# Optimization experiments

Measured on AMD Instinct MI355X. Metric: run time of the kernel, lower is better.

Reference implementation:

```python
import jax, jax.numpy as jnp
import numpy as np

# Renderer constants matching neural_renderer.Renderer(camera_mode='look',
# light_intensity_ambient=0.5, light_intensity_directional=0.5,
# light_direction=[0,0,1], viewing_angle=45) with image_size=256.
IMG = 256
TEX = 6
VIEW_ANGLE_DEG = 45.0
EYE = np.array([0.0, 0.0, -2.0], dtype=np.float32)          # camera position (look mode)
CAM_DIR = np.array([0.0, 0.0, 1.0], dtype=np.float32)       # camera_direction
CAM_UP = np.array([0.0, 1.0, 0.0], dtype=np.float32)        # camera_up
LIGHT_DIR = np.array([0.0, 0.0, 1.0], dtype=np.float32)
AMBIENT = 0.5
DIRECTIONAL = 0.5
EPS = 1e-8


def setup_inputs() -> dict:
    key = jax.random.key(0)
    k1, k2, k3 = jax.random.split(key, 3)
    # mesh roughly centered at origin; camera sits at z=-2 looking toward +z
    vertices = 0.5 * jax.random.normal(k1, (1, 400, 3), dtype=jnp.float32)
    faces = jax.random.randint(k2, (1, 640, 3), 0, 400, dtype=jnp.int64)
    textures = 0.5 * jax.random.normal(k3, (1, 640, TEX, TEX, TEX, 3), dtype=jnp.float32)
    return {"vertices": vertices, "faces": faces, "textures": textures}


def _normalize(v):
    return v / (jnp.linalg.norm(v, axis=-1, keepdims=True) + EPS)


def reference(vertices, faces, textures):
    v = vertices[0]                 # [N,3]
    f = faces[0]                    # [F,3] int
    tex = jnp.tanh(textures[0])     # [F,T,T,T,3]  (torch.tanh(textures))

    fv = v[f]                       # [F,3,3] per-face vertex positions (world)

    # ---- lighting (ambient + directional, white lights) ----
    n = jnp.cross(fv[:, 1] - fv[:, 0], fv[:, 2] - fv[:, 0])  # [F,3]
    n = _normalize(n)
    diff = jax.nn.relu(n @ jnp.asarray(LIGHT_DIR))           # [F]
    light = AMBIENT + DIRECTIONAL * diff                     # [F] (same for rgb)

    # ---- 'look' camera transform ----
    z_ax = _normalize(jnp.asarray(CAM_DIR))
    x_ax = _normalize(jnp.cross(jnp.asarray(CAM_UP), z_ax))
    y_ax = jnp.cross(z_ax, x_ax)
    R = jnp.stack([x_ax, y_ax, z_ax], axis=0)                # [3,3]
    vc = (fv - jnp.asarray(EYE)) @ R.T                       # [F,3,3] camera space

    # ---- perspective projection ----
    wfov = jnp.tan(jnp.deg2rad(VIEW_ANGLE_DEG)).astype(jnp.float32)
    zc = vc[..., 2]                                          # [F,3] depth
    xy = vc[..., :2] / (zc[..., None] * wfov + EPS)          # [F,3,2] in [-1,1]

    # ---- rasterize: barycentric coords per pixel per face ----
    ps = (jnp.arange(IMG, dtype=jnp.float32) + 0.5) / IMG * 2.0 - 1.0
    px, py = jnp.meshgrid(ps, -ps, indexing="xy")            # image y flipped
    pts = jnp.stack([px.ravel(), py.ravel()], axis=-1)       # [P,2]

    v0 = xy[:, 0]                                            # [F,2]
    d = xy[:, 1] - v0                                        # [F,2]
    e = xy[:, 2] - v0                                        # [F,2]
    det = d[:, 0] * e[:, 1] - d[:, 1] * e[:, 0]              # [F]
    det_ok = jnp.abs(det) > 1e-8
    det_s = jnp.where(det_ok, det, 1.0)

    q = pts[:, None, :] - v0[None, :, :]                     # [P,F,2]
    w1 = (q[..., 0] * e[:, 1] - q[..., 1] * e[:, 0]) / det_s # [P,F]
    w2 = (d[:, 0] * q[..., 1] - d[:, 1] * q[..., 0]) / det_s # [P,F]
    w0 = 1.0 - w1 - w2

    inside = (w0 >= 0) & (w1 >= 0) & (w2 >= 0) & det_ok[None, :]
    depth = w0 * zc[:, 0] + w1 * zc[:, 1] + w2 * zc[:, 2]    # [P,F]
    visible = inside & (depth > 0)

    # ---- z-buffer: nearest visible face per pixel ----
    big = jnp.float32(1e30)
    dmask = jnp.where(visible, depth, big)                   # [P,F]
    idx = jnp.argmin(dmask, axis=1)                          # [P]
    valid = jnp.take_along_axis(visible, idx[:, None], axis=1)[:, 0]  # [P]

    gather = lambda a: jnp.take_along_axis(a, idx[:, None], axis=1)[:, 0]
    b0, b1, b2 = gather(w0), gather(w1), gather(w2)          # [P] each

    # ---- texture lookup: nearest cell in TxTxT cube by barycentric coords ----
    ti = lambda b: jnp.clip((b * TEX).astype(jnp.int32), 0, TEX - 1)
    i0, i1, i2 = ti(b0), ti(b1), ti(b2)
    col = tex[idx, i0, i1, i2]                               # [P,3]
    col = col * light[idx][:, None]                          # shade

    img = jnp.where(valid[:, None], col, 0.0)                # [P,3]
    img = img.reshape(IMG, IMG, 3).transpose(2, 0, 1)[None]  # [1,3,H,W]
    return img
```

## Files before the change

kernel.cpp:

```cpp
#include <hip/hip_runtime.h>
#include <math.h>

#define NF   640
#define IMGN 256
#define NPIX (IMGN * IMGN)
#define TEXN 6
#define TPB  512
#define PXW  64
#define NCH  8
#define CHF  (NF / NCH)

__global__ __launch_bounds__(TPB) void render_kernel(
    const float* __restrict__ verts,
    const int*   __restrict__ faces,
    const float* __restrict__ tex,
    float* __restrict__ out)
{
#pragma clang fp contract(off)
    __shared__ float4 fA[NF];
    __shared__ float4 fB[NF];
    __shared__ float2 fZ[NF];
    __shared__ unsigned short sList[NCH][CHF];
    __shared__ float rD[NCH][PXW];
    __shared__ int   rI[NCH][PXW];

    const float EPSf = 1e-8f;
    const int tid  = (int)threadIdx.x;
    const int wid  = tid >> 6;
    const int lane = tid & 63;
    const int p0   = (int)blockIdx.x * PXW;
    const int pi   = p0 >> 8;
    const int pj0  = p0 & (IMGN - 1);

    const float by    = -(((pi + 0.5f) / (float)IMGN) * 2.0f - 1.0f);
    const float bxmin = ((pj0 + 0.5f) / (float)IMGN) * 2.0f - 1.0f;
    const float bxmax = ((pj0 + (PXW - 1) + 0.5f) / (float)IMGN) * 2.0f - 1.0f;

    const int fbeg = wid * CHF;
    int cnt = 0;
    for (int r = 0; r < 2; ++r) {
        int idx = r * 64 + lane;
        int f = fbeg + idx;
        bool pred = false;
        if (idx < CHF) {
            int ia = faces[3 * f + 0];
            int ib = faces[3 * f + 1];
            int ic = faces[3 * f + 2];
            float ax = verts[3 * ia], ay = verts[3 * ia + 1], az = verts[3 * ia + 2];
            float bx = verts[3 * ib], byy = verts[3 * ib + 1], bz = verts[3 * ib + 2];
            float cx = verts[3 * ic], cy = verts[3 * ic + 1], cz = verts[3 * ic + 2];

            float z0 = az + 2.0f, z1 = bz + 2.0f, z2 = cz + 2.0f;
            float den0 = z0 * 1.0f + EPSf;
            float den1 = z1 * 1.0f + EPSf;
            float den2 = z2 * 1.0f + EPSf;
            float px0 = ax / den0, py0 = ay / den0;
            float px1 = bx / den1, py1 = byy / den1;
            float px2 = cx / den2, py2 = cy / den2;

            float dx = px1 - px0, dy = py1 - py0;
            float ex = px2 - px0, ey = py2 - py0;
            float det = dx * ey - dy * ex;
            bool ok = fabsf(det) > 1e-8f;

            fA[f] = make_float4(px0, py0, ex, ey);
            fB[f] = make_float4(dx, dy, ok ? det : 1.0f, z0);
            fZ[f] = make_float2(z1, z2);

            if (ok) {
                float xmin = fminf(px0, fminf(px1, px2));
                float xmax = fmaxf(px0, fmaxf(px1, px2));
                float ymin = fminf(py0, fminf(py1, py2));
                float ymax = fmaxf(py0, fmaxf(py1, py2));
                float padx = (fmaxf(fabsf(xmin), fabsf(xmax)) + 1.0f) * 1e-6f;
                float pady = (fmaxf(fabsf(ymin), fabsf(ymax)) + 1.0f) * 1e-6f;
                pred = (ymin - pady <= by)    && (ymax + pady >= by) &&
                       (xmin - padx <= bxmax) && (xmax + padx >= bxmin);
            }
        }
        unsigned long long m = __ballot(pred);
        if (pred)
            sList[wid][cnt + (int)__popcll(m & ((1ull << lane) - 1ull))] =
                (unsigned short)f;
        cnt += (int)__popcll(m);
    }

    const float ppx = ((pj0 + lane + 0.5f) / (float)IMGN) * 2.0f - 1.0f;
    const float ppy = by;

    float best = 1e30f;
    int   bi = -1;

    for (int k = 0; k < cnt; ++k) {
        int f = (int)sList[wid][k];
        float4 a = fA[f];
        float4 b = fB[f];
        float qx = ppx - a.x;
        float qy = ppy - a.y;
        float n1 = qx * a.w - qy * a.z;
        float n2 = b.x * qy - b.y * qx;
        bool pass = (b.z > 0.0f) ? (n1 >= 0.0f && n2 >= 0.0f)
                                 : (n1 <= 0.0f && n2 <= 0.0f);
        if (pass) {
            float w1 = n1 / b.z;
            float w2 = n2 / b.z;
            float w0 = (1.0f - w1) - w2;
            if (w0 >= 0.0f) {
                float2 zz = fZ[f];
                float depth = ((w0 * b.w) + (w1 * zz.x)) + (w2 * zz.y);
                if (depth > 0.0f && depth < best) {
                    best = depth; bi = f;
                }
            }
        }
    }

    rD[wid][lane] = best;
    rI[wid][lane] = bi;
    __syncthreads();

    if (tid < PXW) {
        float bd = rD[0][tid];
        int   fi = rI[0][tid];
        for (int c = 1; c < NCH; ++c) {
            float d = rD[c][tid];
            if (d < bd) { bd = d; fi = rI[c][tid]; }
        }

        int pp = p0 + tid;
        float r = 0.0f, g = 0.0f, b = 0.0f;
        if (fi >= 0) {
            float4 a2 = fA[fi];
            float4 b2 = fB[fi];
            float sx = ((pj0 + tid + 0.5f) / (float)IMGN) * 2.0f - 1.0f;
            float qx = sx - a2.x;
            float qy = by - a2.y;
            float n1 = qx * a2.w - qy * a2.z;
            float n2 = b2.x * qy - b2.y * qx;
            float w1 = n1 / b2.z;
            float w2 = n2 / b2.z;
            float w0 = (1.0f - w1) - w2;

            int ia = faces[3 * fi + 0];
            int ib = faces[3 * fi + 1];
            int ic = faces[3 * fi + 2];
            float ax = verts[3 * ia], ay = verts[3 * ia + 1], az = verts[3 * ia + 2];
            float bx = verts[3 * ib], byv = verts[3 * ib + 1], bz = verts[3 * ib + 2];
            float cx = verts[3 * ic], cy = verts[3 * ic + 1], cz = verts[3 * ic + 2];
            float e1x = bx - ax, e1y = byv - ay, e1z = bz - az;
            float e2x = cx - ax, e2y = cy - ay, e2z = cz - az;
            float nx = e1y * e2z - e1z * e2y;
            float ny = e1z * e2x - e1x * e2z;
            float nz = e1x * e2y - e1y * e2x;
            float nn = sqrtf((nx * nx + ny * ny) + nz * nz) + EPSf;
            float diff = nz / nn;
            diff = diff > 0.0f ? diff : 0.0f;
            float light = 0.5f + 0.5f * diff;

            int i0 = (int)(w0 * (float)TEXN);
            int i1 = (int)(w1 * (float)TEXN);
            int i2 = (int)(w2 * (float)TEXN);
            i0 = i0 < 0 ? 0 : (i0 > TEXN - 1 ? TEXN - 1 : i0);
            i1 = i1 < 0 ? 0 : (i1 > TEXN - 1 ? TEXN - 1 : i1);
            i2 = i2 < 0 ? 0 : (i2 > TEXN - 1 ? TEXN - 1 : i2);
            const float* tp = tex + (size_t)((((fi * TEXN + i0) * TEXN + i1) * TEXN + i2) * 3);
            r = tanhf(tp[0]) * light;
            g = tanhf(tp[1]) * light;
            b = tanhf(tp[2]) * light;
        }
        out[pp]            = r;
        out[NPIX + pp]     = g;
        out[2 * NPIX + pp] = b;
    }
}

extern "C" void kernel_launch(void* const* d_in, const int* in_sizes, int n_in,
                              void* d_out, int out_size, void* d_ws, size_t ws_size,
                              hipStream_t stream) {
    (void)in_sizes; (void)n_in; (void)d_ws; (void)ws_size; (void)out_size;
    const float* verts = (const float*)d_in[0];
    const int*   faces = (const int*)d_in[1];
    const float* tex   = (const float*)d_in[2];
    float*       out   = (float*)d_out;
    render_kernel<<<NPIX / PXW, TPB, 0, stream>>>(verts, faces, tex, out);
}
```

Measured before the change: 26.17 us.

## Process two pixels per lane and stage vertices in shared memory

Doubles the pixel strip per block to 128, so each lane tests two pixels against every face in its list. This halves the number of blocks that each redo the per-face setup and culling, and shares the face loads and row-dependent terms between the two pixels. Vertices are copied into shared memory once per block so the setup and shading gathers avoid scattered global loads. The trade-off is fewer blocks (512), which lowers parallelism and GPU fill, plus an extra barrier.

```diff
diff --git a/kernel.cpp b/kernel.cpp
--- a/kernel.cpp
+++ b/kernel.cpp
@@ -6,9 +6,10 @@
 #define NPIX (IMGN * IMGN)
 #define TEXN 6
 #define TPB  512
-#define PXW  64
+#define PXW  128
 #define NCH  8
 #define CHF  (NF / NCH)
+#define NVF  1200
 
 __global__ __launch_bounds__(TPB) void render_kernel(
     const float* __restrict__ verts,
@@ -17,6 +18,7 @@
     float* __restrict__ out)
 {
 #pragma clang fp contract(off)
+    __shared__ float  sV[NVF];
     __shared__ float4 fA[NF];
     __shared__ float4 fB[NF];
     __shared__ float2 fZ[NF];
@@ -35,6 +37,9 @@
     const float by    = -(((pi + 0.5f) / (float)IMGN) * 2.0f - 1.0f);
     const float bxmin = ((pj0 + 0.5f) / (float)IMGN) * 2.0f - 1.0f;
     const float bxmax = ((pj0 + (PXW - 1) + 0.5f) / (float)IMGN) * 2.0f - 1.0f;
+
+    for (int i = tid; i < NVF; i += TPB) sV[i] = verts[i];
+    __syncthreads();
 
     const int fbeg = wid * CHF;
     int cnt = 0;
@@ -46,9 +51,9 @@
             int ia = faces[3 * f + 0];
             int ib = faces[3 * f + 1];
             int ic = faces[3 * f + 2];
-            float ax = verts[3 * ia], ay = verts[3 * ia + 1], az = verts[3 * ia + 2];
-            float bx = verts[3 * ib], byy = verts[3 * ib + 1], bz = verts[3 * ib + 2];
-            float cx = verts[3 * ic], cy = verts[3 * ic + 1], cz = verts[3 * ic + 2];
+            float ax = sV[3 * ia], ay = sV[3 * ia + 1], az = sV[3 * ia + 2];
+            float bx = sV[3 * ib], byy = sV[3 * ib + 1], bz = sV[3 * ib + 2];
+            float cx = sV[3 * ic], cy = sV[3 * ic + 1], cz = sV[3 * ic + 2];
 
             float z0 = az + 2.0f, z1 = bz + 2.0f, z2 = cz + 2.0f;
             float den0 = z0 * 1.0f + EPSf;
@@ -85,38 +90,60 @@
         cnt += (int)__popcll(m);
     }
 
-    const float ppx = ((pj0 + lane + 0.5f) / (float)IMGN) * 2.0f - 1.0f;
-    const float ppy = by;
-
-    float best = 1e30f;
-    int   bi = -1;
+    const float ppx0 = ((pj0 + lane      + 0.5f) / (float)IMGN) * 2.0f - 1.0f;
+    const float ppx1 = ((pj0 + lane + 64 + 0.5f) / (float)IMGN) * 2.0f - 1.0f;
+
+    float best0 = 1e30f, best1 = 1e30f;
+    int   bi0 = -1,      bi1 = -1;
 
     for (int k = 0; k < cnt; ++k) {
         int f = (int)sList[wid][k];
         float4 a = fA[f];
         float4 b = fB[f];
-        float qx = ppx - a.x;
-        float qy = ppy - a.y;
-        float n1 = qx * a.w - qy * a.z;
-        float n2 = b.x * qy - b.y * qx;
-        bool pass = (b.z > 0.0f) ? (n1 >= 0.0f && n2 >= 0.0f)
-                                 : (n1 <= 0.0f && n2 <= 0.0f);
-        if (pass) {
-            float w1 = n1 / b.z;
-            float w2 = n2 / b.z;
-            float w0 = (1.0f - w1) - w2;
-            if (w0 >= 0.0f) {
-                float2 zz = fZ[f];
-                float depth = ((w0 * b.w) + (w1 * zz.x)) + (w2 * zz.y);
-                if (depth > 0.0f && depth < best) {
-                    best = depth; bi = f;
+        float2 zz = fZ[f];
+        float qy = by - a.y;
+        float t1 = qy * a.z;
+        float t2 = b.x * qy;
+        bool detpos = (b.z > 0.0f);
+
+        {
+            float qx = ppx0 - a.x;
+            float n1 = qx * a.w - t1;
+            float n2 = t2 - b.y * qx;
+            bool pass = detpos ? (n1 >= 0.0f && n2 >= 0.0f)
+                               : (n1 <= 0.0f && n2 <= 0.0f);
+            if (pass) {
+                float w1 = n1 / b.z;
+                float w2 = n2 / b.z;
+                float w0 = (1.0f - w1) - w2;
+                if (w0 >= 0.0f) {
+                    float depth = ((w0 * b.w) + (w1 * zz.x)) + (w2 * zz.y);
+                    if (depth > 0.0f && depth < best0) { best0 = depth; bi0 = f; }
                 }
             }
         }
+        {
+            float qx = ppx1 - a.x;
+            float n1 = qx * a.w - t1;
+            float n2 = t2 - b.y * qx;
+            bool pass = detpos ? (n1 >= 0.0f && n2 >= 0.0f)
+                               : (n1 <= 0.0f && n2 <= 0.0f);
+            if (pass) {
+                float w1 = n1 / b.z;
+                float w2 = n2 / b.z;
+                float w0 = (1.0f - w1) - w2;
+                if (w0 >= 0.0f) {
+                    float depth = ((w0 * b.w) + (w1 * zz.x)) + (w2 * zz.y);
+                    if (depth > 0.0f && depth < best1) { best1 = depth; bi1 = f; }
+                }
+            }
+        }
     }
 
-    rD[wid][lane] = best;
-    rI[wid][lane] = bi;
+    rD[wid][lane]      = best0;
+    rI[wid][lane]      = bi0;
+    rD[wid][lane + 64] = best1;
+    rI[wid][lane + 64] = bi1;
     __syncthreads();
 
     if (tid < PXW) {
@@ -144,9 +171,9 @@
             int ia = faces[3 * fi + 0];
             int ib = faces[3 * fi + 1];
             int ic = faces[3 * fi + 2];
-            float ax = verts[3 * ia], ay = verts[3 * ia + 1], az = verts[3 * ia + 2];
-            float bx = verts[3 * ib], byv = verts[3 * ib + 1], bz = verts[3 * ib + 2];
-            float cx = verts[3 * ic], cy = verts[3 * ic + 1], cz = verts[3 * ic + 2];
+            float ax = sV[3 * ia], ay = sV[3 * ia + 1], az = sV[3 * ia + 2];
+            float bx = sV[3 * ib], byv = sV[3 * ib + 1], bz = sV[3 * ib + 2];
+            float cx = sV[3 * ic], cy = sV[3 * ic + 1], cz = sV[3 * ic + 2];
             float e1x = bx - ax, e1y = byv - ay, e1z = bz - az;
             float e2x = cx - ax, e2y = cy - ay, e2z = cz - az;
             float nx = e1y * e2z - e1z * e2y;
```

Measured after the change: 30.22 us. +15.5%, slower.

## Cache projected vertices in LDS and rebalance face lists across waves

Applied to the files above, without the earlier changes.

Each vertex is now projected once into shared memory, so faces read their corners from there instead of loading and dividing per face corner. The per-wave candidate face lists are merged into one list and split evenly across the eight waves, which removes the imbalance where one wave finishes its list long after the others. This costs two extra block barriers and a small amount of extra shared memory. Because the per-wave min merge is order-independent, the result should be unchanged apart from tie-breaking order.

```diff
diff --git a/kernel.cpp b/kernel.cpp
--- a/kernel.cpp
+++ b/kernel.cpp
@@ -5,6 +5,7 @@
 #define IMGN 256
 #define NPIX (IMGN * IMGN)
 #define TEXN 6
+#define NV   400
 #define TPB  512
 #define PXW  64
 #define NCH  8
@@ -17,10 +18,13 @@
     float* __restrict__ out)
 {
 #pragma clang fp contract(off)
+    __shared__ float  sPX[NV], sPY[NV], sZ[NV];
     __shared__ float4 fA[NF];
     __shared__ float4 fB[NF];
     __shared__ float2 fZ[NF];
-    __shared__ unsigned short sList[NCH][CHF];
+    __shared__ unsigned short sListW[NCH][CHF];
+    __shared__ unsigned short sMerged[NF];
+    __shared__ int   sCnt[NCH];
     __shared__ float rD[NCH][PXW];
     __shared__ int   rI[NCH][PXW];
 
@@ -35,6 +39,16 @@
     const float by    = -(((pi + 0.5f) / (float)IMGN) * 2.0f - 1.0f);
     const float bxmin = ((pj0 + 0.5f) / (float)IMGN) * 2.0f - 1.0f;
     const float bxmax = ((pj0 + (PXW - 1) + 0.5f) / (float)IMGN) * 2.0f - 1.0f;
+
+    if (tid < NV) {
+        float x = verts[3 * tid], y = verts[3 * tid + 1], z = verts[3 * tid + 2];
+        float z0 = z + 2.0f;
+        float den = z0 * 1.0f + EPSf;
+        sPX[tid] = x / den;
+        sPY[tid] = y / den;
+        sZ[tid]  = z0;
+    }
+    __syncthreads();
 
     const int fbeg = wid * CHF;
     int cnt = 0;
@@ -46,17 +60,9 @@
             int ia = faces[3 * f + 0];
             int ib = faces[3 * f + 1];
             int ic = faces[3 * f + 2];
-            float ax = verts[3 * ia], ay = verts[3 * ia + 1], az = verts[3 * ia + 2];
-            float bx = verts[3 * ib], byy = verts[3 * ib + 1], bz = verts[3 * ib + 2];
-            float cx = verts[3 * ic], cy = verts[3 * ic + 1], cz = verts[3 * ic + 2];
-
-            float z0 = az + 2.0f, z1 = bz + 2.0f, z2 = cz + 2.0f;
-            float den0 = z0 * 1.0f + EPSf;
-            float den1 = z1 * 1.0f + EPSf;
-            float den2 = z2 * 1.0f + EPSf;
-            float px0 = ax / den0, py0 = ay / den0;
-            float px1 = bx / den1, py1 = byy / den1;
-            float px2 = cx / den2, py2 = cy / den2;
+            float px0 = sPX[ia], py0 = sPY[ia], z0 = sZ[ia];
+            float px1 = sPX[ib], py1 = sPY[ib], z1 = sZ[ib];
+            float px2 = sPX[ic], py2 = sPY[ic], z2 = sZ[ic];
 
             float dx = px1 - px0, dy = py1 - py0;
             float ex = px2 - px0, ey = py2 - py0;
@@ -80,19 +86,36 @@
         }
         unsigned long long m = __ballot(pred);
         if (pred)
-            sList[wid][cnt + (int)__popcll(m & ((1ull << lane) - 1ull))] =
+            sListW[wid][cnt + (int)__popcll(m & ((1ull << lane) - 1ull))] =
                 (unsigned short)f;
         cnt += (int)__popcll(m);
     }
+    if (lane == 0) sCnt[wid] = cnt;
+    __syncthreads();
+
+    int base = 0, total = 0;
+    #pragma unroll
+    for (int c = 0; c < NCH; ++c) {
+        int cc = sCnt[c];
+        if (c < wid) base += cc;
+        total += cc;
+    }
+    for (int i = lane; i < cnt; i += 64)
+        sMerged[base + i] = sListW[wid][i];
+    __syncthreads();
 
     const float ppx = ((pj0 + lane + 0.5f) / (float)IMGN) * 2.0f - 1.0f;
     const float ppy = by;
 
+    const int per = (total + NCH - 1) >> 3;
+    const int kb  = wid * per;
+    const int ke  = (kb + per < total) ? (kb + per) : total;
+
     float best = 1e30f;
     int   bi = -1;
 
-    for (int k = 0; k < cnt; ++k) {
-        int f = (int)sList[wid][k];
+    for (int k = kb; k < ke; ++k) {
+        int f = (int)sMerged[k];
         float4 a = fA[f];
         float4 b = fB[f];
         float qx = ppx - a.x;
```

After: 25.49 us. 1.03x faster.
